# Kernel tuning notes

Hardware: AMD Instinct MI355X
Metric: run time of the kernel (lower is better)

## Reference

```python
import jax, jax.numpy as jnp
import numpy as np

N, D, C = 16384, 1024, 1024
EPS = 1e-6       # F.pairwise_distance eps added to the difference
DENOM_EPS = 1e-5


def setup_inputs() -> dict:
    key = jax.random.key(0)
    k1, k2, k3 = jax.random.split(key, 3)
    features = jax.random.normal(k1, (N, D), dtype=jnp.float32)
    labels = jax.random.randint(k2, (N,), 0, 10, dtype=jnp.int64)
    centers = jax.random.normal(k3, (C, D), dtype=jnp.float32)
    return {"features": features, "labels": labels, "centers": centers}


def reference(features, labels, centers):
    # torch: dist = ||f - c + eps||_2 per (sample, center) pair.
    # Expand exactly: ||f - c + eps||^2 = ||f||^2 + ||c||^2 - 2 f.c
    #                 + 2*eps*(sum(f) - sum(c)) + eps^2 * D
    f2 = jnp.sum(features * features, axis=1)            # [N]
    c2 = jnp.sum(centers * centers, axis=1)              # [C]
    fc = features @ centers.T                            # [N, C]
    fs = jnp.sum(features, axis=1)                       # [N]
    cs = jnp.sum(centers, axis=1)                        # [C]
    d = features.shape[1]
    sq = (f2[:, None] + c2[None, :] - 2.0 * fc
          + 2.0 * EPS * (fs[:, None] - cs[None, :]) + (EPS * EPS) * d)
    dist = jnp.sqrt(jnp.maximum(sq, 0.0))                # [N, C]
    min_dist = jnp.min(dist, axis=1)                     # [N]
    mask = (labels == 0).astype(min_dist.dtype)          # select label==0 samples
    count = jnp.sum(mask)
    loss = jnp.sum(min_dist * mask) / (count + DENOM_EPS)
    return loss
```

## Files before the change

### kernel.cpp

```cpp
#include <hip/hip_runtime.h>


constexpr int N = 16384;
constexpr int D = 1024;
constexpr int C = 1024;
constexpr float EPS = 1e-6f;

constexpr int SB = 16;
constexpr int CB = 128;
constexpr int BK = 64;
constexpr int TPB = 256;
constexpr int DIST_GRID = 1024;

typedef __attribute__((ext_vector_type(8))) short bf16x8;
typedef __attribute__((ext_vector_type(4))) float f32x4;

__device__ inline unsigned mapf(float f) {
  unsigned b = __float_as_uint(f);
  return (b & 0x80000000u) ? ~b : (b | 0x80000000u);
}
__device__ inline float unmapf(unsigned u) {
  return __uint_as_float((u & 0x80000000u) ? (u ^ 0x80000000u) : ~u);
}

__device__ inline unsigned short f2bf(float x) {
  unsigned u = __float_as_uint(x);
  return (unsigned short)((u + 0x7FFFu + ((u >> 16) & 1u)) >> 16);
}

#define GLOAD_LDS16(gp, lp)                                        \
  __builtin_amdgcn_global_load_lds(                                \
      (const __attribute__((address_space(1))) void*)(gp),         \
      (__attribute__((address_space(3))) void*)(lp), 16, 0, 0)

__global__ __launch_bounds__(TPB) void k_setup(
    const float* __restrict__ feat, const int* __restrict__ labels,
    const float* __restrict__ cent, unsigned* __restrict__ count,
    unsigned* __restrict__ sel, unsigned* __restrict__ minmapped,
    float* __restrict__ cc, float* __restrict__ ff,
    unsigned short* __restrict__ cent_bf) {
  __shared__ float red[8];
  __shared__ unsigned lrow[16], lslot[16];
  __shared__ int lcount;

  const int b = blockIdx.x, t = threadIdx.x;
  const int lane = t & 63, w = t >> 6;

  if (t == 0) lcount = 0;
  __syncthreads();

  if (t < 16) {
    int n = b * 16 + t;
    minmapped[n] = 0xFFFFFFFFu;
    if (labels[n] == 0) {
      unsigned slot = atomicAdd(count, 1u);
      sel[slot] = (unsigned)n;
      int li = atomicAdd(&lcount, 1);
      lrow[li] = (unsigned)n;
      lslot[li] = slot;
    }
  }

  {
    const float* row = cent + (size_t)b * D;
    float4 v = *(const float4*)(row + t * 4);
    *(short4*)(cent_bf + (size_t)b * D + t * 4) =
        make_short4((short)f2bf(v.x), (short)f2bf(v.y), (short)f2bf(v.z),
                    (short)f2bf(v.w));
    float s1 = v.x + v.y + v.z + v.w;
    float s2 = v.x * v.x + v.y * v.y + v.z * v.z + v.w * v.w;
#pragma unroll
    for (int off = 32; off; off >>= 1) {
      s1 += __shfl_down(s1, off);
      s2 += __shfl_down(s2, off);
    }
    if (lane == 0) { red[w] = s1; red[4 + w] = s2; }
    __syncthreads();
    if (t == 0) {
      float a1 = red[0] + red[1] + red[2] + red[3];
      float a2 = red[4] + red[5] + red[6] + red[7];
      cc[b] = a2 - 2.0f * EPS * a1;
    }
  }

  const int nl = lcount;
  for (int i = 0; i < nl; ++i) {
    __syncthreads();
    const float* row = feat + (size_t)lrow[i] * D;
    float4 v = *(const float4*)(row + t * 4);
    float s1 = v.x + v.y + v.z + v.w;
    float s2 = v.x * v.x + v.y * v.y + v.z * v.z + v.w * v.w;
#pragma unroll
    for (int off = 32; off; off >>= 1) {
      s1 += __shfl_down(s1, off);
      s2 += __shfl_down(s2, off);
    }
    if (lane == 0) { red[w] = s1; red[4 + w] = s2; }
    __syncthreads();
    if (t == 0) {
      float a1 = red[0] + red[1] + red[2] + red[3];
      float a2 = red[4] + red[5] + red[6] + red[7];
      ff[lslot[i]] = a2 + 2.0f * EPS * a1 + EPS * EPS * (float)D;
    }
  }
}

__global__ __launch_bounds__(TPB) void k_dist(
    const float* __restrict__ feat, const unsigned short* __restrict__ cent_bf,
    const float* __restrict__ cc, const unsigned* __restrict__ count,
    const unsigned* __restrict__ sel, unsigned* __restrict__ minmapped) {
  __shared__ __align__(16) unsigned short Cb[CB * BK];
  __shared__ __align__(16) unsigned short Fb[SB * BK];
  __shared__ unsigned rows_s[SB];

  const unsigned cnt = *count;
  const unsigned nwork = ((cnt + SB - 1) / SB) * (C / CB);

  const int t = threadIdx.x;
  const int lane = t & 63, w = t >> 6;

  const int fs_ = t >> 4;
  const int fk4 = (t & 15) * 4;
  const int fj = fk4 >> 3, fhalf = (fk4 >> 2) & 1;
  const int foff = fs_ * BK + ((fj ^ (fs_ & 7)) << 3) + (fhalf << 2);
  const int arow = lane & 15, kg = lane >> 4;
  const int c0 = w * 32 + (lane & 15), c1 = c0 + 16;

  for (unsigned wk = blockIdx.x; wk < nwork; wk += DIST_GRID) {
    const unsigned sbase = (wk >> 3) * SB;
    const unsigned cbase = (wk & 7) * CB;

    if (t < SB) rows_s[t] = sel[min(sbase + (unsigned)t, cnt - 1u)];
    __syncthreads();

    const float* fsrc = feat + (size_t)rows_s[fs_] * D + fk4;
    f32x4 acc0 = {0.f, 0.f, 0.f, 0.f}, acc1 = {0.f, 0.f, 0.f, 0.f};

    for (int kt = 0; kt < D / BK; ++kt) {
      const int kbase = kt * BK;
#pragma unroll
      for (int u = 0; u < 4; ++u) {
        int chunk = (w * 4 + u) * 64 + lane;
        int r = chunk >> 3, j = chunk & 7;
        int jsrc = j ^ (r & 7);
        const unsigned short* src =
            cent_bf + (size_t)(cbase + r) * D + kbase + jsrc * 8;
        GLOAD_LDS16(src, Cb + chunk * 8);
      }
      {
        float4 v = *(const float4*)(fsrc + kbase);
        *(short4*)(Fb + foff) = make_short4((short)f2bf(v.x), (short)f2bf(v.y),
                                            (short)f2bf(v.z), (short)f2bf(v.w));
      }
      __syncthreads();

#pragma unroll
      for (int ks = 0; ks < 2; ++ks) {
        int jj = (ks << 2) + kg;
        bf16x8 a = *(const bf16x8*)(Fb + arow * BK + ((jj ^ (arow & 7)) << 3));
        bf16x8 b0 = *(const bf16x8*)(Cb + c0 * BK + ((jj ^ (c0 & 7)) << 3));
        bf16x8 b1 = *(const bf16x8*)(Cb + c1 * BK + ((jj ^ (c1 & 7)) << 3));
        acc0 = __builtin_amdgcn_mfma_f32_16x16x32_bf16(a, b0, acc0, 0, 0, 0);
        acc1 = __builtin_amdgcn_mfma_f32_16x16x32_bf16(a, b1, acc1, 0, 0, 0);
      }
      __syncthreads();
    }

    float ccv0 = cc[cbase + c0];
    float ccv1 = cc[cbase + c1];
#pragma unroll
    for (int reg = 0; reg < 4; ++reg) {
      float v = fminf(ccv0 - 2.0f * acc0[reg], ccv1 - 2.0f * acc1[reg]);
#pragma unroll
      for (int off = 1; off < 16; off <<= 1) v = fminf(v, __shfl_xor(v, off));
      if ((lane & 15) == 0) {
        unsigned sidx = sbase + (unsigned)((lane >> 4) * 4 + reg);
        if (sidx < cnt) atomicMin(&minmapped[sidx], mapf(v));
      }
    }
    __syncthreads();
  }
}

__global__ __launch_bounds__(TPB) void k_final_out(
    const unsigned* __restrict__ count, const float* __restrict__ ff,
    const unsigned* __restrict__ minmapped, float* __restrict__ num,
    unsigned* __restrict__ done, float* __restrict__ out) {
  const unsigned cnt = *count;
  const int t = threadIdx.x;
  const int lane = t & 63;

  float s = 0.f;
  for (unsigned i = blockIdx.x * TPB + t; i < cnt; i += gridDim.x * TPB) {
    float sq = ff[i] + unmapf(minmapped[i]);
    s += sqrtf(fmaxf(sq, 0.0f));
  }
#pragma unroll
  for (int off = 32; off; off >>= 1) s += __shfl_down(s, off);
  if (lane == 0) atomicAdd(num, s);

  __syncthreads();
  if (t == 0) {
    __threadfence();
    unsigned v = atomicAdd(done, 1u);
    if (v == gridDim.x - 1u) {
      float total = atomicAdd(num, 0.0f);
      out[0] = total / ((float)cnt + 1e-5f);
    }
  }
}

extern "C" void kernel_launch(void* const* d_in, const int* in_sizes, int n_in,
                              void* d_out, int out_size, void* d_ws, size_t ws_size,
                              hipStream_t stream) {
  const float* feat = (const float*)d_in[0];
  const int* labels = (const int*)d_in[1];
  const float* cent = (const float*)d_in[2];
  float* out = (float*)d_out;

  char* ws = (char*)d_ws;
  unsigned* count = (unsigned*)ws;
  float* num = (float*)(ws + 4);
  unsigned* done = (unsigned*)(ws + 8);
  unsigned* minmapped = (unsigned*)(ws + 16);
  unsigned* sel = (unsigned*)(ws + 16 + 4 * (size_t)N);
  float* cc = (float*)(ws + 16 + 8 * (size_t)N);
  float* ff = (float*)(ws + 16 + 8 * (size_t)N + 4 * (size_t)C);
  unsigned short* cent_bf =
      (unsigned short*)(ws + 16 + 12 * (size_t)N + 4 * (size_t)C);

  hipMemsetAsync(d_ws, 0, 16, stream);

  k_setup<<<1024, TPB, 0, stream>>>(feat, labels, cent, count, sel, minmapped,
                                    cc, ff, cent_bf);
  k_dist<<<DIST_GRID, TPB, 0, stream>>>(feat, cent_bf, cc, count, sel,
                                        minmapped);
  k_final_out<<<32, TPB, 0, stream>>>(count, ff, minmapped, num, done, out);
}
```

Baseline: 140.1 us.

## Double-buffer LDS tiles in k_dist and fuse final reduction via last-block

The distance GEMM loop now uses two LDS buffers so the next K-tile's centre and feature loads are issued while the current tile's MFMAs run, cutting the exposed load latency of the single-buffer scheme. The separate final reduction kernel is removed: the last block to finish k_dist, found with an atomic counter, computes the masked sqrt-sum and writes the loss, saving one kernel launch. LDS use doubles, which can lower occupancy, and the fused tail runs serially in one block.

```diff
diff --git a/kernel.cpp b/kernel.cpp
--- a/kernel.cpp
+++ b/kernel.cpp
@@ -9,6 +9,7 @@
 constexpr int SB = 16;
 constexpr int CB = 128;
 constexpr int BK = 64;
+constexpr int NKT = D / BK;
 constexpr int TPB = 256;
 constexpr int DIST_GRID = 1024;
 
@@ -108,10 +109,14 @@
 __global__ __launch_bounds__(TPB) void k_dist(
     const float* __restrict__ feat, const unsigned short* __restrict__ cent_bf,
     const float* __restrict__ cc, const unsigned* __restrict__ count,
-    const unsigned* __restrict__ sel, unsigned* __restrict__ minmapped) {
-  __shared__ __align__(16) unsigned short Cb[CB * BK];
-  __shared__ __align__(16) unsigned short Fb[SB * BK];
+    const unsigned* __restrict__ sel, unsigned* __restrict__ minmapped,
+    const float* __restrict__ ff, unsigned* __restrict__ done,
+    float* __restrict__ out) {
+  __shared__ __align__(16) unsigned short Cb[2][CB * BK];
+  __shared__ __align__(16) unsigned short Fb[2][SB * BK];
   __shared__ unsigned rows_s[SB];
+  __shared__ float red[4];
+  __shared__ unsigned amlast;
 
   const unsigned cnt = *count;
   const unsigned nwork = ((cnt + SB - 1) / SB) * (C / CB);
@@ -136,7 +141,7 @@
     const float* fsrc = feat + (size_t)rows_s[fs_] * D + fk4;
     f32x4 acc0 = {0.f, 0.f, 0.f, 0.f}, acc1 = {0.f, 0.f, 0.f, 0.f};
 
-    for (int kt = 0; kt < D / BK; ++kt) {
+    auto stage = [&](int kt, int bb) {
       const int kbase = kt * BK;
 #pragma unroll
       for (int u = 0; u < 4; ++u) {
@@ -145,21 +150,28 @@
         int jsrc = j ^ (r & 7);
         const unsigned short* src =
             cent_bf + (size_t)(cbase + r) * D + kbase + jsrc * 8;
-        GLOAD_LDS16(src, Cb + chunk * 8);
+        GLOAD_LDS16(src, &Cb[bb][chunk * 8]);
       }
-      {
-        float4 v = *(const float4*)(fsrc + kbase);
-        *(short4*)(Fb + foff) = make_short4((short)f2bf(v.x), (short)f2bf(v.y),
+      float4 v = *(const float4*)(fsrc + kbase);
+      *(short4*)&Fb[bb][foff] = make_short4((short)f2bf(v.x), (short)f2bf(v.y),
                                             (short)f2bf(v.z), (short)f2bf(v.w));
-      }
-      __syncthreads();
-
+    };
+
+    stage(0, 0);
+    __syncthreads();
+
+    for (int kt = 0; kt < NKT; ++kt) {
+      const int cur = kt & 1;
+      if (kt + 1 < NKT) stage(kt + 1, cur ^ 1);
 #pragma unroll
       for (int ks = 0; ks < 2; ++ks) {
         int jj = (ks << 2) + kg;
-        bf16x8 a = *(const bf16x8*)(Fb + arow * BK + ((jj ^ (arow & 7)) << 3));
-        bf16x8 b0 = *(const bf16x8*)(Cb + c0 * BK + ((jj ^ (c0 & 7)) << 3));
-        bf16x8 b1 = *(const bf16x8*)(Cb + c1 * BK + ((jj ^ (c1 & 7)) << 3));
+        bf16x8 a =
+            *(const bf16x8*)&Fb[cur][arow * BK + ((jj ^ (arow & 7)) << 3)];
+        bf16x8 b0 =
+            *(const bf16x8*)&Cb[cur][c0 * BK + ((jj ^ (c0 & 7)) << 3)];
+        bf16x8 b1 =
+            *(const bf16x8*)&Cb[cur][c1 * BK + ((jj ^ (c1 & 7)) << 3)];
         acc0 = __builtin_amdgcn_mfma_f32_16x16x32_bf16(a, b0, acc0, 0, 0, 0);
         acc1 = __builtin_amdgcn_mfma_f32_16x16x32_bf16(a, b1, acc1, 0, 0, 0);
       }
@@ -180,31 +192,24 @@
     }
     __syncthreads();
   }
-}
-
-__global__ __launch_bounds__(TPB) void k_final_out(
-    const unsigned* __restrict__ count, const float* __restrict__ ff,
-    const unsigned* __restrict__ minmapped, float* __restrict__ num,
-    unsigned* __restrict__ done, float* __restrict__ out) {
-  const unsigned cnt = *count;
-  const int t = threadIdx.x;
-  const int lane = t & 63;
-
-  float s = 0.f;
-  for (unsigned i = blockIdx.x * TPB + t; i < cnt; i += gridDim.x * TPB) {
-    float sq = ff[i] + unmapf(minmapped[i]);
-    s += sqrtf(fmaxf(sq, 0.0f));
-  }
-#pragma unroll
-  for (int off = 32; off; off >>= 1) s += __shfl_down(s, off);
-  if (lane == 0) atomicAdd(num, s);
-
-  __syncthreads();
+
   if (t == 0) {
     __threadfence();
-    unsigned v = atomicAdd(done, 1u);
-    if (v == gridDim.x - 1u) {
-      float total = atomicAdd(num, 0.0f);
+    amlast = (atomicAdd(done, 1u) == (unsigned)gridDim.x - 1u) ? 1u : 0u;
+  }
+  __syncthreads();
+  if (amlast) {
+    float s = 0.f;
+    for (unsigned i = (unsigned)t; i < cnt; i += TPB) {
+      float sq = ff[i] + unmapf(atomicAdd(&minmapped[i], 0u));
+      s += sqrtf(fmaxf(sq, 0.0f));
+    }
+#pragma unroll
+    for (int off = 32; off; off >>= 1) s += __shfl_down(s, off);
+    if (lane == 0) red[w] = s;
+    __syncthreads();
+    if (t == 0) {
+      float total = red[0] + red[1] + red[2] + red[3];
       out[0] = total / ((float)cnt + 1e-5f);
     }
   }
@@ -220,7 +225,6 @@
 
   char* ws = (char*)d_ws;
   unsigned* count = (unsigned*)ws;
-  float* num = (float*)(ws + 4);
   unsigned* done = (unsigned*)(ws + 8);
   unsigned* minmapped = (unsigned*)(ws + 16);
   unsigned* sel = (unsigned*)(ws + 16 + 4 * (size_t)N);
@@ -234,6 +238,5 @@
   k_setup<<<1024, TPB, 0, stream>>>(feat, labels, cent, count, sel, minmapped,
                                     cc, ff, cent_bf);
   k_dist<<<DIST_GRID, TPB, 0, stream>>>(feat, cent_bf, cc, count, sel,
-                                        minmapped);
-  k_final_out<<<32, TPB, 0, stream>>>(count, ff, minmapped, num, done, out);
-}
+                                        minmapped, ff, done, out);
+}
```

After: 156.6 us. 11.8% more time.
